# Kernel optimization log

Hardware: AMD Instinct MI355X
Metric: run time of the kernel (lower is better)

## Reference

```python
import jax, jax.numpy as jnp
import numpy as np

T, N, F, H, C, E = 8, 50000, 128, 64, 4, 800000


def setup_inputs() -> dict:
    key = jax.random.key(0)
    ks = jax.random.split(key, 8)
    x = jax.random.normal(ks[0], (T, N, F), jnp.float32)
    edges = jax.random.randint(ks[1], (T, 2, E), 0, N, jnp.int32)
    # GCNConv weights (one per timestep, glorot-ish scale) + Linear layers
    Wg = jax.random.normal(ks[2], (T, F, H), jnp.float32) / np.sqrt(F)
    bg = jnp.zeros((T, H), jnp.float32)
    W1 = jax.random.normal(ks[3], (H, 32), jnp.float32) / np.sqrt(H)
    b1 = jnp.zeros((32,), jnp.float32)
    W2 = jax.random.normal(ks[4], (32, 16), jnp.float32) / np.sqrt(32)
    b2 = jnp.zeros((16,), jnp.float32)
    W3 = jax.random.normal(ks[5], (16, C), jnp.float32) / np.sqrt(16)
    b3 = jnp.zeros((C,), jnp.float32)
    return dict(x=x, edges=edges, Wg=Wg, bg=bg, W1=W1, b1=b1, W2=W2, b2=b2, W3=W3, b3=b3)


def gcn_conv(x, edge_index, W, b):
    """PyG GCNConv: add self-loops, sym-normalized aggregation of x @ W, plus bias."""
    n = x.shape[0]
    loop = jnp.arange(n, dtype=edge_index.dtype)
    src = jnp.concatenate([edge_index[0], loop])  # message sources
    dst = jnp.concatenate([edge_index[1], loop])  # aggregation targets
    deg = jax.ops.segment_sum(jnp.ones_like(dst, dtype=x.dtype), dst, num_segments=n)
    dinv = jnp.where(deg > 0, jax.lax.rsqrt(deg), 0.0)
    xw = x @ W                                    # [n, H]
    norm = (dinv[src] * dinv[dst])[:, None]       # [E+n, 1]
    out = jax.ops.segment_sum(xw[src] * norm, dst, num_segments=n)
    return out + b


def reference(x, edges, Wg, bg, W1, b1, W2, b2, W3, b3):
    def step(acc, inp):
        xt, et, Wt, bt = inp
        return acc + jax.nn.relu(gcn_conv(xt, et, Wt, bt)), None

    acc0 = jnp.zeros((x.shape[1], Wg.shape[-1]), x.dtype)
    h, _ = jax.lax.scan(step, acc0, (x, edges, Wg, bg))  # sum over T timesteps
    h = jax.nn.relu(h)                 # dropout omitted (eval mode)
    h = jax.nn.relu(h @ W1 + b1)
    h = jax.nn.relu(h @ W2 + b2)
    logits = h @ W3 + b3
    return jax.nn.log_softmax(logits, axis=1)
```

## Files before the change

kernel.cpp:

```cpp
#include <hip/hip_runtime.h>
#include <hip/hip_bf16.h>

#define TT 8
#define NN 50000
#define FF 128
#define HH 64
#define CC 4
#define EE 800000
#define NB2 391
#define CAP 2560
#define BPT 64

typedef unsigned short u16;
typedef unsigned int u32;
typedef __attribute__((ext_vector_type(8))) short bf16x8;
typedef __attribute__((ext_vector_type(4))) float f32x4;

static __device__ __forceinline__ float bflo(u32 w) {
    union { unsigned int i; float f; } v; v.i = w << 16; return v.f;
}
static __device__ __forceinline__ float bfhi(u32 w) {
    union { unsigned int i; float f; } v; v.i = w & 0xFFFF0000u; return v.f;
}
static __device__ __forceinline__ u16 cvt_bf16(float f) {
    __hip_bfloat16 b = __float2bfloat16(f);
    return *reinterpret_cast<u16*>(&b);
}

__global__ __launch_bounds__(256) void multisplit_kernel(const int* __restrict__ edges,
                                                         int* __restrict__ gcur, u32* __restrict__ binned) {
    __shared__ u32 sbuf[NB2][16];
    __shared__ int scnt[NB2];
    int bid = blockIdx.x;
    int t = bid & 7;
    int blk = bid >> 3;
    const int per = (EE + BPT - 1) / BPT;
    int e0 = blk * per;
    int e1 = e0 + per; if (e1 > EE) e1 = EE;

    for (int i = threadIdx.x; i < NB2; i += 256) scnt[i] = 0;
    __syncthreads();

    const int* es = edges + (size_t)(t * 2 + 0) * EE;
    const int* ed = edges + (size_t)(t * 2 + 1) * EE;
    int* gc = gcur + t * NB2;
    u32* bb = binned + (size_t)t * NB2 * CAP;

    for (int base = e0; base < e1; base += 512) {
        u32 recA = 0, recB = 0; int bA = -1, bB = -1;
        int eA = base + threadIdx.x;
        int eB = base + 256 + threadIdx.x;
        if (eA < e1) {
            int src = es[eA], dst = ed[eA];
            bA = dst >> 7;
            recA = (u32)src | ((u32)(dst & 127) << 16);
            int p = atomicAdd(&scnt[bA], 1);
            if (p < 16) { sbuf[bA][p] = recA; bA = -1; }
        }
        if (eB < e1) {
            int src = es[eB], dst = ed[eB];
            bB = dst >> 7;
            recB = (u32)src | ((u32)(dst & 127) << 16);
            int p = atomicAdd(&scnt[bB], 1);
            if (p < 16) { sbuf[bB][p] = recB; bB = -1; }
        }
        __syncthreads();
        for (int fb = threadIdx.x; fb < NB2; fb += 256) {
            if (scnt[fb] >= 16) {
                int g = atomicAdd(&gc[fb], 16);
                uint4* dp = (uint4*)(bb + (size_t)fb * CAP + g);
                uint4* sp = (uint4*)&sbuf[fb][0];
                dp[0] = sp[0]; dp[1] = sp[1]; dp[2] = sp[2]; dp[3] = sp[3];
                scnt[fb] = 0;
            }
        }
        __syncthreads();
        if (bA >= 0) {
            int p = atomicAdd(&scnt[bA], 1);
            if (p < 16) sbuf[bA][p] = recA;
            else { int g = atomicAdd(&gc[bA], 1); bb[(size_t)bA * CAP + g] = recA; }
        }
        if (bB >= 0) {
            int p = atomicAdd(&scnt[bB], 1);
            if (p < 16) sbuf[bB][p] = recB;
            else { int g = atomicAdd(&gc[bB], 1); bb[(size_t)bB * CAP + g] = recB; }
        }
        __syncthreads();
    }
    for (int fb = threadIdx.x; fb < NB2; fb += 256) {
        int c = scnt[fb];
        if (c > 0) {
            int g = atomicAdd(&gc[fb], c);
            for (int k = 0; k < c; ++k) bb[(size_t)fb * CAP + g + k] = sbuf[fb][k];
        }
    }
}

__global__ __launch_bounds__(256) void csr_scatter_kernel(const u32* __restrict__ binned, const int* __restrict__ gcur,
                                                          u16* __restrict__ srclist, u32* __restrict__ nodeinfo,
                                                          float* __restrict__ dinv) {
    __shared__ u32 recs[CAP];
    __shared__ int hist[128];
    __shared__ int cur[128];
    int b = blockIdx.x, t = blockIdx.y, tid = threadIdx.x;
    int node0 = b * 128;
    int tot = gcur[t * NB2 + b];
    const u32* win = binned + ((size_t)t * NB2 + b) * CAP;

    for (int i = tid; i < tot; i += 256) recs[i] = win[i];
    if (tid < 128) hist[tid] = 0;
    __syncthreads();
    for (int i = tid; i < tot; i += 256) atomicAdd(&hist[recs[i] >> 16], 1);
    __syncthreads();
    int h = 0;
    if (tid < 128) h = hist[tid];
    for (int off = 1; off < 128; off <<= 1) {
        int v = 0;
        if (tid < 128 && tid >= off) v = hist[tid - off];
        __syncthreads();
        if (tid < 128) hist[tid] += v;
        __syncthreads();
    }
    if (tid < 128) {
        int excl = hist[tid] - h;
        cur[tid] = excl;
        int node = node0 + tid;
        if (node < NN) {
            nodeinfo[t * NN + node] = (u32)(b * CAP + excl) | ((u32)h << 20);
            dinv[t * NN + node] = rsqrtf(1.0f + (float)h);
        }
    }
    __syncthreads();
    u16* sl = srclist + (size_t)t * NB2 * CAP;
    for (int i = tid; i < tot; i += 256) {
        u32 rec = recs[i];
        int d = rec >> 16;
        int p = atomicAdd(&cur[d], 1);
        sl[(size_t)b * CAP + p] = (u16)(rec & 0xFFFF);
    }
}

__global__ __launch_bounds__(256) void wt_prep_kernel(const float* __restrict__ Wg, u16* __restrict__ wt) {
    int t = blockIdx.x;
    const float* w = Wg + t * FF * HH;
    u16* o = wt + (size_t)t * HH * FF;
    for (int i = threadIdx.x; i < FF * HH; i += 256) {
        int k = i >> 6, c = i & 63;
        o[c * FF + k] = cvt_bf16(w[i]);
    }
}

__global__ __launch_bounds__(256) void xw_kernel(const float* __restrict__ x, const u16* __restrict__ wt,
                                                 const float* __restrict__ dinv, u16* __restrict__ y) {
    int t = blockIdx.y;
    int row0 = blockIdx.x * 128;
    int tid = threadIdx.x;
    int w = tid >> 6, lane = tid & 63;
    int l15 = lane & 15, lg = lane >> 4;
    __shared__ __align__(16) u16 ylds[128][72];
    const float* xt = x + (size_t)t * NN * FF;
    const u16* wtt = wt + (size_t)t * HH * FF;

    f32x4 d[2][4] = {{{0,0,0,0},{0,0,0,0},{0,0,0,0},{0,0,0,0}},
                     {{0,0,0,0},{0,0,0,0},{0,0,0,0},{0,0,0,0}}};
    #pragma unroll
    for (int k0 = 0; k0 < 128; k0 += 32) {
        int kb = k0 + lg * 8;
        union { bf16x8 v; __hip_bfloat162 h[4]; } au[2];
        #pragma unroll
        for (int s = 0; s < 2; ++s) {
            int arow = row0 + w * 32 + s * 16 + l15;
            if (arow < NN) {
                float4 f0 = *reinterpret_cast<const float4*>(&xt[(size_t)arow * FF + kb]);
                float4 f1 = *reinterpret_cast<const float4*>(&xt[(size_t)arow * FF + kb + 4]);
                au[s].h[0] = __float22bfloat162_rn(make_float2(f0.x, f0.y));
                au[s].h[1] = __float22bfloat162_rn(make_float2(f0.z, f0.w));
                au[s].h[2] = __float22bfloat162_rn(make_float2(f1.x, f1.y));
                au[s].h[3] = __float22bfloat162_rn(make_float2(f1.z, f1.w));
            } else {
                au[s].v = (bf16x8){0,0,0,0,0,0,0,0};
            }
        }
        #pragma unroll
        for (int n = 0; n < 4; ++n) {
            bf16x8 bf = *reinterpret_cast<const bf16x8*>(&wtt[(size_t)(n * 16 + l15) * FF + kb]);
            d[0][n] = __builtin_amdgcn_mfma_f32_16x16x32_bf16(au[0].v, bf, d[0][n], 0, 0, 0);
            d[1][n] = __builtin_amdgcn_mfma_f32_16x16x32_bf16(au[1].v, bf, d[1][n], 0, 0, 0);
        }
    }
    #pragma unroll
    for (int s = 0; s < 2; ++s) {
        int rl = w * 32 + s * 16 + lg * 4;
        float dv[4];
        #pragma unroll
        for (int i = 0; i < 4; ++i) {
            int grow = row0 + rl + i;
            dv[i] = (grow < NN) ? dinv[t * NN + grow] : 0.f;
        }
        #pragma unroll
        for (int n = 0; n < 4; ++n) {
            int col = n * 16 + l15;
            #pragma unroll
            for (int i = 0; i < 4; ++i)
                ylds[rl + i][col] = cvt_bf16(d[s][n][i] * dv[i]);
        }
    }
    __syncthreads();
    u16* yt = y + (size_t)t * NN * HH;
    #pragma unroll
    for (int it = 0; it < 4; ++it) {
        int idx = it * 256 + tid;
        int r = idx >> 3, c8 = (idx & 7) * 8;
        int grow = row0 + r;
        if (grow < NN)
            *reinterpret_cast<uint4*>(&yt[(size_t)grow * HH + c8]) =
                *reinterpret_cast<const uint4*>(&ylds[r][c8]);
    }
}

__global__ __launch_bounds__(256) void agg_kernel(const u16* __restrict__ y, const float* __restrict__ dinv,
                                                  const u32* __restrict__ nodeinfo, const u16* __restrict__ srclist,
                                                  const float* __restrict__ bg, float* __restrict__ acc) {
    int node = blockIdx.x * 4 + (threadIdx.x >> 6);
    int lane = threadIdx.x & 63;
    int sub = lane >> 4;
    int fo = lane & 15;
    float a0 = 0.f, a1 = 0.f, a2 = 0.f, a3 = 0.f;
    for (int t = 0; t < TT; ++t) {
        const u16* yt = y + (size_t)t * NN * HH;
        u32 info = nodeinfo[t * NN + node];
        int cnt = info >> 20;
        const u16* sl = srclist + (size_t)t * NB2 * CAP + (info & 0xFFFFF);
        float s0 = 0.f, s1 = 0.f, s2 = 0.f, s3 = 0.f;
        int j = 0;
        for (; j + 16 <= cnt; j += 16) {
            int e0 = sl[j + sub], e1 = sl[j + 4 + sub], e2 = sl[j + 8 + sub], e3 = sl[j + 12 + sub];
            uint2 v0 = *reinterpret_cast<const uint2*>(&yt[(size_t)e0 * HH + fo * 4]);
            uint2 v1 = *reinterpret_cast<const uint2*>(&yt[(size_t)e1 * HH + fo * 4]);
            uint2 v2 = *reinterpret_cast<const uint2*>(&yt[(size_t)e2 * HH + fo * 4]);
            uint2 v3 = *reinterpret_cast<const uint2*>(&yt[(size_t)e3 * HH + fo * 4]);
            s0 += (bflo(v0.x) + bflo(v1.x)) + (bflo(v2.x) + bflo(v3.x));
            s1 += (bfhi(v0.x) + bfhi(v1.x)) + (bfhi(v2.x) + bfhi(v3.x));
            s2 += (bflo(v0.y) + bflo(v1.y)) + (bflo(v2.y) + bflo(v3.y));
            s3 += (bfhi(v0.y) + bfhi(v1.y)) + (bfhi(v2.y) + bfhi(v3.y));
        }
        for (; j < cnt; j += 4) {
            int e = j + sub;
            uint2 v = make_uint2(0u, 0u);
            if (e < cnt) {
                int srcid = sl[e];
                v = *reinterpret_cast<const uint2*>(&yt[(size_t)srcid * HH + fo * 4]);
            }
            s0 += bflo(v.x);
            s1 += bfhi(v.x);
            s2 += bflo(v.y);
            s3 += bfhi(v.y);
        }
        s0 += __shfl_xor(s0, 16, 64); s0 += __shfl_xor(s0, 32, 64);
        s1 += __shfl_xor(s1, 16, 64); s1 += __shfl_xor(s1, 32, 64);
        s2 += __shfl_xor(s2, 16, 64); s2 += __shfl_xor(s2, 32, 64);
        s3 += __shfl_xor(s3, 16, 64); s3 += __shfl_xor(s3, 32, 64);
        uint2 sv = *reinterpret_cast<const uint2*>(&yt[(size_t)node * HH + fo * 4]);
        s0 += bflo(sv.x);
        s1 += bfhi(sv.x);
        s2 += bflo(sv.y);
        s3 += bfhi(sv.y);
        float dvv = dinv[t * NN + node];
        float4 bgv = *reinterpret_cast<const float4*>(&bg[t * HH + fo * 4]);
        a0 += fmaxf(dvv * s0 + bgv.x, 0.f);
        a1 += fmaxf(dvv * s1 + bgv.y, 0.f);
        a2 += fmaxf(dvv * s2 + bgv.z, 0.f);
        a3 += fmaxf(dvv * s3 + bgv.w, 0.f);
    }
    if (sub == 0) {
        float4 o = make_float4(a0, a1, a2, a3);
        *reinterpret_cast<float4*>(&acc[(size_t)node * HH + fo * 4]) = o;
    }
}

__global__ __launch_bounds__(256) void head_kernel(const float* __restrict__ acc,
                                                   const float* __restrict__ W1, const float* __restrict__ b1,
                                                   const float* __restrict__ W2, const float* __restrict__ b2,
                                                   const float* __restrict__ W3, const float* __restrict__ b3,
                                                   float* __restrict__ out) {
    __shared__ float w1[64 * 32], w2[32 * 16], w3[16 * 4], bb1[32], bb2[16], bb3[4];
    int tid = threadIdx.x;
    for (int i = tid; i < 2048; i += 256) w1[i] = W1[i];
    for (int i = tid; i < 512; i += 256) w2[i] = W2[i];
    if (tid < 64) w3[tid] = W3[tid];
    if (tid < 32) bb1[tid] = b1[tid];
    if (tid < 16) bb2[tid] = b2[tid];
    if (tid < 4) bb3[tid] = b3[tid];
    __syncthreads();
    int node = blockIdx.x * 256 + tid;
    if (node >= NN) return;

    float a[64];
    #pragma unroll
    for (int k = 0; k < 64; ++k) a[k] = acc[(size_t)node * HH + k];

    float h1[32];
    for (int j = 0; j < 32; ++j) {
        float s = bb1[j];
        #pragma unroll
        for (int k = 0; k < 64; ++k) s += a[k] * w1[k * 32 + j];
        h1[j] = fmaxf(s, 0.f);
    }
    float h2[16];
    for (int j = 0; j < 16; ++j) {
        float s = bb2[j];
        #pragma unroll
        for (int k = 0; k < 32; ++k) s += h1[k] * w2[k * 16 + j];
        h2[j] = fmaxf(s, 0.f);
    }
    float l[4];
    for (int c = 0; c < 4; ++c) {
        float s = bb3[c];
        #pragma unroll
        for (int k = 0; k < 16; ++k) s += h2[k] * w3[k * 4 + c];
        l[c] = s;
    }
    float m = fmaxf(fmaxf(l[0], l[1]), fmaxf(l[2], l[3]));
    float sum = 0.f;
    #pragma unroll
    for (int c = 0; c < 4; ++c) sum += expf(l[c] - m);
    float lse = logf(sum);
    float4 o;
    o.x = l[0] - m - lse; o.y = l[1] - m - lse; o.z = l[2] - m - lse; o.w = l[3] - m - lse;
    *reinterpret_cast<float4*>(&out[(size_t)node * CC]) = o;
}

extern "C" void kernel_launch(void* const* d_in, const int* in_sizes, int n_in,
                              void* d_out, int out_size, void* d_ws, size_t ws_size,
                              hipStream_t stream) {
    const float* x    = (const float*)d_in[0];
    const int*  edges = (const int*)d_in[1];
    const float* Wg   = (const float*)d_in[2];
    const float* bg   = (const float*)d_in[3];
    const float* W1   = (const float*)d_in[4];
    const float* b1   = (const float*)d_in[5];
    const float* W2   = (const float*)d_in[6];
    const float* b2   = (const float*)d_in[7];
    const float* W3   = (const float*)d_in[8];
    const float* b3   = (const float*)d_in[9];
    float* out = (float*)d_out;

    char* ws = (char*)d_ws;
    size_t o = 0;
    int* gcur      = (int*)(ws + o); o += (size_t)TT * NB2 * 4;
    o = (o + 255) & ~(size_t)255;
    float* dinv    = (float*)(ws + o); o += (size_t)TT * NN * 4;
    u32* nodeinfo  = (u32*)(ws + o); o += (size_t)TT * NN * 4;
    o = (o + 255) & ~(size_t)255;
    u16* wt        = (u16*)(ws + o); o += (size_t)TT * HH * FF * 2;
    o = (o + 255) & ~(size_t)255;
    u32* binned    = (u32*)(ws + o); o += (size_t)TT * NB2 * CAP * 4;
    u16* srclist   = (u16*)(ws + o); o += (size_t)TT * NB2 * CAP * 2;
    u16* y         = (u16*)(ws + o); o += (size_t)TT * NN * HH * 2;
    float* acc     = (float*)(ws + o); o += (size_t)NN * HH * 4;

    hipMemsetAsync(gcur, 0, (size_t)TT * NB2 * 4, stream);

    multisplit_kernel<<<BPT * TT, 256, 0, stream>>>(edges, gcur, binned);

    dim3 gsc(NB2, TT);
    csr_scatter_kernel<<<gsc, 256, 0, stream>>>(binned, gcur, srclist, nodeinfo, dinv);

    wt_prep_kernel<<<TT, 256, 0, stream>>>(Wg, wt);

    dim3 gx(NB2, TT);
    xw_kernel<<<gx, 256, 0, stream>>>(x, wt, dinv, y);

    agg_kernel<<<12500, 256, 0, stream>>>(y, dinv, nodeinfo, srclist, bg, acc);

    head_kernel<<<196, 256, 0, stream>>>(acc, W1, b1, W2, b2, W3, b3, out);
}
```

Before: 366.9 us.

## Retune multisplit blocks, shuffle-scan CSR offsets, enlarge xw tiles, split aggregation

Doubles the multisplit blocks per timestep. The CSR scatter's barrier-heavy shared-memory scan becomes a single-wavefront shuffle scan over node pairs. The xw GEMM uses 512-thread blocks covering 256 rows. Aggregation is split into two launches over timestep halves, with the second reading back the partial accumulator, which likely improves cache locality of the gathered y rows at the cost of an extra read/write of acc.

```diff
diff --git a/kernel.cpp b/kernel.cpp
--- a/kernel.cpp
+++ b/kernel.cpp
@@ -9,7 +9,7 @@
 #define EE 800000
 #define NB2 391
 #define CAP 2560
-#define BPT 64
+#define BPT 128
 
 typedef unsigned short u16;
 typedef unsigned int u32;
@@ -112,22 +112,26 @@
     __syncthreads();
     for (int i = tid; i < tot; i += 256) atomicAdd(&hist[recs[i] >> 16], 1);
     __syncthreads();
-    int h = 0;
-    if (tid < 128) h = hist[tid];
-    for (int off = 1; off < 128; off <<= 1) {
-        int v = 0;
-        if (tid < 128 && tid >= off) v = hist[tid - off];
-        __syncthreads();
-        if (tid < 128) hist[tid] += v;
-        __syncthreads();
-    }
-    if (tid < 128) {
-        int excl = hist[tid] - h;
-        cur[tid] = excl;
-        int node = node0 + tid;
+    if (tid < 64) {
+        int v0 = hist[2 * tid], v1 = hist[2 * tid + 1];
+        int pair = v0 + v1;
+        int inc = pair;
+        #pragma unroll
+        for (int off = 1; off < 64; off <<= 1) {
+            int u = __shfl_up(inc, off, 64);
+            if (tid >= off) inc += u;
+        }
+        int exclp = inc - pair;
+        cur[2 * tid] = exclp;
+        cur[2 * tid + 1] = exclp + v0;
+        int node = node0 + 2 * tid;
         if (node < NN) {
-            nodeinfo[t * NN + node] = (u32)(b * CAP + excl) | ((u32)h << 20);
-            dinv[t * NN + node] = rsqrtf(1.0f + (float)h);
+            nodeinfo[t * NN + node] = (u32)(b * CAP + exclp) | ((u32)v0 << 20);
+            dinv[t * NN + node] = rsqrtf(1.0f + (float)v0);
+        }
+        if (node + 1 < NN) {
+            nodeinfo[t * NN + node + 1] = (u32)(b * CAP + exclp + v0) | ((u32)v1 << 20);
+            dinv[t * NN + node + 1] = rsqrtf(1.0f + (float)v1);
         }
     }
     __syncthreads();
@@ -150,14 +154,14 @@
     }
 }
 
-__global__ __launch_bounds__(256) void xw_kernel(const float* __restrict__ x, const u16* __restrict__ wt,
+__global__ __launch_bounds__(512) void xw_kernel(const float* __restrict__ x, const u16* __restrict__ wt,
                                                  const float* __restrict__ dinv, u16* __restrict__ y) {
     int t = blockIdx.y;
-    int row0 = blockIdx.x * 128;
+    int row0 = blockIdx.x * 256;
     int tid = threadIdx.x;
     int w = tid >> 6, lane = tid & 63;
     int l15 = lane & 15, lg = lane >> 4;
-    __shared__ __align__(16) u16 ylds[128][72];
+    __shared__ __align__(16) u16 ylds[256][72];
     const float* xt = x + (size_t)t * NN * FF;
     const u16* wtt = wt + (size_t)t * HH * FF;
 
@@ -209,7 +213,7 @@
     u16* yt = y + (size_t)t * NN * HH;
     #pragma unroll
     for (int it = 0; it < 4; ++it) {
-        int idx = it * 256 + tid;
+        int idx = it * 512 + tid;
         int r = idx >> 3, c8 = (idx & 7) * 8;
         int grow = row0 + r;
         if (grow < NN)
@@ -220,13 +224,20 @@
 
 __global__ __launch_bounds__(256) void agg_kernel(const u16* __restrict__ y, const float* __restrict__ dinv,
                                                   const u32* __restrict__ nodeinfo, const u16* __restrict__ srclist,
-                                                  const float* __restrict__ bg, float* __restrict__ acc) {
+                                                  const float* __restrict__ bg, float* __restrict__ acc,
+                                                  int t0, int t1, int first) {
     int node = blockIdx.x * 4 + (threadIdx.x >> 6);
     int lane = threadIdx.x & 63;
     int sub = lane >> 4;
     int fo = lane & 15;
-    float a0 = 0.f, a1 = 0.f, a2 = 0.f, a3 = 0.f;
-    for (int t = 0; t < TT; ++t) {
+    float a0, a1, a2, a3;
+    if (first) {
+        a0 = a1 = a2 = a3 = 0.f;
+    } else {
+        float4 pv = *reinterpret_cast<const float4*>(&acc[(size_t)node * HH + fo * 4]);
+        a0 = pv.x; a1 = pv.y; a2 = pv.z; a3 = pv.w;
+    }
+    for (int t = t0; t < t1; ++t) {
         const u16* yt = y + (size_t)t * NN * HH;
         u32 info = nodeinfo[t * NN + node];
         int cnt = info >> 20;
@@ -368,10 +379,11 @@
 
     wt_prep_kernel<<<TT, 256, 0, stream>>>(Wg, wt);
 
-    dim3 gx(NB2, TT);
-    xw_kernel<<<gx, 256, 0, stream>>>(x, wt, dinv, y);
-
-    agg_kernel<<<12500, 256, 0, stream>>>(y, dinv, nodeinfo, srclist, bg, acc);
+    dim3 gx(196, TT);
+    xw_kernel<<<gx, 512, 0, stream>>>(x, wt, dinv, y);
+
+    agg_kernel<<<12500, 256, 0, stream>>>(y, dinv, nodeinfo, srclist, bg, acc, 0, 4, 1);
+    agg_kernel<<<12500, 256, 0, stream>>>(y, dinv, nodeinfo, srclist, bg, acc, 4, 8, 0);
 
     head_kernel<<<196, 256, 0, stream>>>(acc, W1, b1, W2, b2, W3, b3, out);
 }
```

Measured after the change: 362.6 us. Within noise of the previous version (-1.2%).
